# Kernel optimization log

Hardware: AMD Instinct MI355X
Metric: run time of the kernel (lower is better)

## Reference

```python
import jax, jax.numpy as jnp
import numpy as np

D_MODEL, D_K, D_V, H, GRID = 512, 64, 64, 8, 196
B = 4


def setup_inputs() -> dict:
    key = jax.random.key(0)
    ks = jax.random.split(key, 12)
    s = 0.02
    return {
        "queries": jax.random.normal(ks[0], (B, GRID, D_MODEL), jnp.float32),
        "keys": jax.random.normal(ks[1], (B, GRID, D_MODEL), jnp.float32),
        "values": jax.random.normal(ks[2], (B, GRID, D_MODEL), jnp.float32),
        "Wq": jax.random.normal(ks[3], (H * D_K, D_MODEL), jnp.float32) * s,
        "bq": jnp.zeros((H * D_K,), jnp.float32),
        "Wk": jax.random.normal(ks[4], (H * D_K, D_MODEL), jnp.float32) * s,
        "bk": jnp.zeros((H * D_K,), jnp.float32),
        "Wv": jax.random.normal(ks[5], (H * D_V, D_MODEL), jnp.float32) * s,
        "bv": jnp.zeros((H * D_V,), jnp.float32),
        "Wo": jax.random.normal(ks[6], (D_MODEL, H * D_V), jnp.float32) * s,
        "bo": jnp.zeros((D_MODEL,), jnp.float32),
        "scale": jnp.ones((1, H, GRID, GRID), jnp.float32) / np.sqrt(D_K).astype(np.float32),
    }


def reference(queries, keys, values, Wq, bq, Wk, bk, Wv, bv, Wo, bo, scale):
    b, nq, _ = queries.shape
    nk = values.shape[1]
    # linear projections (torch nn.Linear: x @ W.T + b)
    q_sig = queries @ Wq.T + bq          # (b, nq, h*dk)
    k_p = keys @ Wk.T + bk               # (b, nk, h*dk)
    v_p = values @ Wv.T + bv             # (b, nk, h*dv)
    # elementwise q*k interaction (b, nq, nk, h*dk)
    att_e = q_sig[:, :, None, :] * k_p[:, None, :, :]
    # sigmoid-gated values
    v_g = jax.nn.sigmoid(att_e) * v_p[:, None, :, :]
    v = v_g.reshape(b, nq, nk, H, D_K).transpose(0, 3, 1, 2, 4)      # (b,h,nq,nk,dk)
    att = att_e.reshape(b, nq, nk, H, D_K).transpose(0, 3, 1, 2, 4)  # (b,h,nq,nk,dk)
    att = att.sum(-1) * scale            # (b,h,nq,nk)
    p = jax.nn.softmax(att, axis=-1)     # dropout is identity in eval mode
    # (att.unsqueeze(-2) @ v).squeeze(-2)
    image = jnp.einsum("bhqk,bhqkd->bhqd", p, v)
    image = image.transpose(0, 2, 1, 3).reshape(b, nq, H * D_V)
    out = image @ Wo.T + bo              # (b, nq, d_model)
    out = jax.nn.sigmoid(q_sig * out) * out
    return out
```

## Files before the change

kernel.cpp:

```cpp
#include <hip/hip_runtime.h>
#include <hip/hip_bf16.h>
#include <math.h>

#define NQ 196
#define BATCH 4
#define HD 512
#define NH 8
#define DK 64
#define MROWS 784
#define MPAD 832

typedef __attribute__((ext_vector_type(8))) short short8;
typedef __attribute__((ext_vector_type(4))) short short4v;
typedef __attribute__((ext_vector_type(4))) float float4v;

__device__ __forceinline__ float b2f(short s) {
  return __uint_as_float(((unsigned)(unsigned short)s) << 16);
}
__device__ __forceinline__ short f2b(float x) {
  return __builtin_bit_cast(short, __float2bfloat16(x));
}
__device__ __forceinline__ float fexp2(float x) {
  float r; asm("v_exp_f32 %0, %1" : "=v"(r) : "v"(x)); return r;
}
__device__ __forceinline__ float frcp(float x) {
  float r; asm("v_rcp_f32 %0, %1" : "=v"(r) : "v"(x)); return r;
}
__device__ __forceinline__ void cvt4(float4 v, short4v& hi, short4v& lo) {
  float x[4] = {v.x, v.y, v.z, v.w};
  #pragma unroll
  for (int i = 0; i < 4; ++i) {
    hi[i] = f2b(x[i]);
    lo[i] = f2b(x[i] - b2f(hi[i]));
  }
}
__device__ __forceinline__ void gload_lds16(const void* g, void* l) {
  __builtin_amdgcn_global_load_lds(
      (const __attribute__((address_space(1))) unsigned int*)g,
      (__attribute__((address_space(3))) unsigned int*)l, 16, 0, 0);
}

struct WSplitArgs { const float* src[7]; short* hi[7]; short* lo[7]; int nblk[7]; };

__global__ __launch_bounds__(256)
void wsplit_kernel(WSplitArgs a) {
  int b = blockIdx.x, seg = 0;
  while (seg < 6 && b >= a.nblk[seg]) { b -= a.nblk[seg]; ++seg; }
  const size_t off = (size_t)b * 2048 + (size_t)threadIdx.x * 8;
  const float* src = a.src[seg] + off;
  float4 v0 = *(const float4*)(src);
  float4 v1 = *(const float4*)(src + 4);
  short4v h0, l0, h1, l1;
  cvt4(v0, h0, l0); cvt4(v1, h1, l1);
  short8 vh = {h0[0],h0[1],h0[2],h0[3],h1[0],h1[1],h1[2],h1[3]};
  short8 vl = {l0[0],l0[1],l0[2],l0[3],l1[0],l1[1],l1[2],l1[3]};
  *(short8*)(a.hi[seg] + off) = vh;
  *(short8*)(a.lo[seg] + off) = vl;
}

struct GemmArgs {
  const short* Ah[3]; const short* Al[3];
  const short* Bh[3]; const short* Bl[3];
  const float* bias[3];
  float* Cf[3]; short* Ch[3]; short* Cl[3]; const float* gate[3];
};

__global__ __launch_bounds__(512)
void mgemm(GemmArgs p, int M, int N, int K) {
  const int z = blockIdx.z;
  const short* __restrict__ Ah = p.Ah[z];
  const short* __restrict__ Al = p.Al[z];
  const short* __restrict__ Bh = p.Bh[z];
  const short* __restrict__ Bl = p.Bl[z];

  __shared__ short smem[32768];
  const int t = threadIdx.x;
  const int ln = t & 63, lm = ln & 15, quad = ln >> 4;
  const int w = t >> 6;
  const int wm = w >> 1, wn = w & 1;
  const int m0 = blockIdx.x << 6, n0 = blockIdx.y << 6;

  const int sr = t >> 3;
  const int sc = ((t & 7) ^ (sr & 7)) << 3;
  const short* gA_h = Ah + (size_t)(m0 + sr) * K + sc;
  const short* gA_l = Al + (size_t)(m0 + sr) * K + sc;
  const short* gB_h = Bh + (size_t)(n0 + sr) * K + sc;
  const short* gB_l = Bl + (size_t)(n0 + sr) * K + sc;
  const int ldst = t * 8;

  float4v acc0 = {0.f,0.f,0.f,0.f}, acc1 = {0.f,0.f,0.f,0.f};

  gload_lds16(gA_h, &smem[0     + ldst]);
  gload_lds16(gA_l, &smem[4096  + ldst]);
  gload_lds16(gB_h, &smem[8192  + ldst]);
  gload_lds16(gB_l, &smem[12288 + ldst]);

  const int NT = K >> 6;
  const int ar = (wm << 4) + lm;
  const int br0 = (wn << 5) + lm, br1 = br0 + 16;
  const int swz = (lm & 7) << 3;

  for (int kt = 0; kt < NT; ++kt) {
    const int buf = kt & 1;
    __syncthreads();
    if (kt + 1 < NT) {
      const int kb = (kt + 1) << 6;
      short* nb = &smem[(buf ^ 1) << 14];
      gload_lds16(gA_h + kb, nb + 0     + ldst);
      gload_lds16(gA_l + kb, nb + 4096  + ldst);
      gload_lds16(gB_h + kb, nb + 8192  + ldst);
      gload_lds16(gB_l + kb, nb + 12288 + ldst);
    }
    const short* Sb = &smem[buf << 14];
    #pragma unroll
    for (int h = 0; h < 2; ++h) {
      const int c = (h << 5) + (quad << 3);
      const int cs = c ^ swz;
      short8 a_h = *(const short8*)&Sb[         ar  * 64 + cs];
      short8 a_l = *(const short8*)&Sb[4096  +  ar  * 64 + cs];
      short8 b0h = *(const short8*)&Sb[8192  +  br0 * 64 + cs];
      short8 b0l = *(const short8*)&Sb[12288 +  br0 * 64 + cs];
      short8 b1h = *(const short8*)&Sb[8192  +  br1 * 64 + cs];
      short8 b1l = *(const short8*)&Sb[12288 +  br1 * 64 + cs];
      acc0 = __builtin_amdgcn_mfma_f32_16x16x32_bf16(a_h, b0h, acc0, 0,0,0);
      acc0 = __builtin_amdgcn_mfma_f32_16x16x32_bf16(a_h, b0l, acc0, 0,0,0);
      acc0 = __builtin_amdgcn_mfma_f32_16x16x32_bf16(a_l, b0h, acc0, 0,0,0);
      acc1 = __builtin_amdgcn_mfma_f32_16x16x32_bf16(a_h, b1h, acc1, 0,0,0);
      acc1 = __builtin_amdgcn_mfma_f32_16x16x32_bf16(a_h, b1l, acc1, 0,0,0);
      acc1 = __builtin_amdgcn_mfma_f32_16x16x32_bf16(a_l, b1h, acc1, 0,0,0);
    }
  }

  const float* bias = p.bias[z];
  const float* gate = p.gate[z];
  float* Cf = p.Cf[z]; short* Ch = p.Ch[z]; short* Cl = p.Cl[z];
  #pragma unroll
  for (int nf = 0; nf < 2; ++nf) {
    const float4v a = nf ? acc1 : acc0;
    const int n = n0 + (wn << 5) + (nf << 4) + lm;
    const float bv = bias[n];
    #pragma unroll
    for (int r = 0; r < 4; ++r) {
      const int m = m0 + (wm << 4) + (quad << 2) + r;
      if (m < M) {
        float c = a[r] + bv;
        if (gate) {
          const float qg = gate[(size_t)m * N + n];
          c = __fdividef(c, 1.f + __expf(-qg * c));
        }
        if (Cf) Cf[(size_t)m * N + n] = c;
        if (Ch) {
          const short hi = f2b(c);
          Ch[(size_t)m * N + n] = hi;
          Cl[(size_t)m * N + n] = f2b(c - b2f(hi));
        }
      }
    }
  }
}

__global__ __launch_bounds__(512)
void attn_fused(const short* __restrict__ qsh, const short* __restrict__ qsl,
                const short* __restrict__ ksh, const short* __restrict__ ksl,
                const float* __restrict__ qsg, const float* __restrict__ kpg,
                const float* __restrict__ vpg, const float* __restrict__ scg,
                short* __restrict__ imgh, short* __restrict__ imgl) {
  const int q0 = blockIdx.x * 16;
  const int h  = blockIdx.y;
  const int b  = blockIdx.z;
  const int t  = threadIdx.x;
  const int w = t >> 6, ln = t & 63;
  const int lm = ln & 15, quad = ln >> 4;
  const float L2E = 1.4426950408889634f;

  __shared__ __align__(16) float S[16][212];
  __shared__ float R[8][16][64];

  const size_t abase = ((size_t)(b * NQ) + q0 + lm) * HD + h * DK + (quad << 3);
  short8 ah0 = *(const short8*)(qsh + abase);
  short8 ah1 = *(const short8*)(qsh + abase + 32);
  short8 al0 = *(const short8*)(qsl + abase);
  short8 al1 = *(const short8*)(qsl + abase + 32);

  for (int nt = w; nt < 13; nt += 8) {
    const size_t bbase = ((size_t)(b * NQ) + nt * 16 + lm) * HD + h * DK + (quad << 3);
    short8 bh0 = *(const short8*)(ksh + bbase);
    short8 bh1 = *(const short8*)(ksh + bbase + 32);
    short8 bl0 = *(const short8*)(ksl + bbase);
    short8 bl1 = *(const short8*)(ksl + bbase + 32);
    float4v acc = {0.f, 0.f, 0.f, 0.f};
    acc = __builtin_amdgcn_mfma_f32_16x16x32_bf16(ah0, bh0, acc, 0,0,0);
    acc = __builtin_amdgcn_mfma_f32_16x16x32_bf16(ah1, bh1, acc, 0,0,0);
    acc = __builtin_amdgcn_mfma_f32_16x16x32_bf16(ah0, bl0, acc, 0,0,0);
    acc = __builtin_amdgcn_mfma_f32_16x16x32_bf16(ah1, bl1, acc, 0,0,0);
    acc = __builtin_amdgcn_mfma_f32_16x16x32_bf16(al0, bh0, acc, 0,0,0);
    acc = __builtin_amdgcn_mfma_f32_16x16x32_bf16(al1, bh1, acc, 0,0,0);
    #pragma unroll
    for (int r = 0; r < 4; ++r)
      S[(quad << 2) + r][nt * 16 + lm] = acc[r];
  }
  __syncthreads();

  for (int i = 0; i < 2; ++i) {
    const int rr = (w << 1) + i;
    const int q = q0 + rr;
    const bool qok = q < NQ;
    const float* srow = scg + ((size_t)h * NQ + (qok ? q : 0)) * NQ;
    float att[4];
    #pragma unroll
    for (int j = 0; j < 4; ++j) {
      const int c = ln + (j << 6);
      att[j] = -1e30f;
      if (c < NQ) att[j] = S[rr][c] * srow[c] * L2E;
    }
    float m = fmaxf(fmaxf(att[0], att[1]), fmaxf(att[2], att[3]));
    #pragma unroll
    for (int off = 32; off; off >>= 1) m = fmaxf(m, __shfl_xor(m, off, 64));
    float e[4], s = 0.f;
    #pragma unroll
    for (int j = 0; j < 4; ++j) { e[j] = fexp2(att[j] - m); s += e[j]; }
    #pragma unroll
    for (int off = 32; off; off >>= 1) s += __shfl_xor(s, off, 64);
    const float rinv = __fdividef(1.f, s);
    #pragma unroll
    for (int j = 0; j < 4; ++j) {
      const int c = ln + (j << 6);
      if (c < NQ) S[rr][c] = e[j] * rinv;
    }
  }
  __syncthreads();

  const int d = ln;
  const int kg = w;
  const int kbeg = kg * 24;
  const int kend = (kg == 7) ? 196 : kbeg + 24;
  const float LOG2E = 1.4426950408889634f;

  float nqs[16];
  #pragma unroll
  for (int qi = 0; qi < 16; ++qi) {
    const int row = min(b * NQ + q0 + qi, MROWS - 1);
    nqs[qi] = -qsg[(size_t)row * HD + h * DK + d] * LOG2E;
  }
  const float* kp = kpg + ((size_t)(b * NQ)) * HD + h * DK + d;
  const float* vp = vpg + ((size_t)(b * NQ)) * HD + h * DK + d;

  float acc[16];
  #pragma unroll
  for (int qi = 0; qi < 16; ++qi) acc[qi] = 0.f;

  for (int k = kbeg; k < kend; k += 4) {
    const float kv0 = kp[(size_t)(k + 0) * HD];
    const float kv1 = kp[(size_t)(k + 1) * HD];
    const float kv2 = kp[(size_t)(k + 2) * HD];
    const float kv3 = kp[(size_t)(k + 3) * HD];
    const float vv0 = vp[(size_t)(k + 0) * HD];
    const float vv1 = vp[(size_t)(k + 1) * HD];
    const float vv2 = vp[(size_t)(k + 2) * HD];
    const float vv3 = vp[(size_t)(k + 3) * HD];
    #pragma unroll
    for (int qi = 0; qi < 16; ++qi) {
      const float4 s4 = *(const float4*)&S[qi][k];
      acc[qi] += s4.x * (vv0 * frcp(1.f + fexp2(nqs[qi] * kv0)));
      acc[qi] += s4.y * (vv1 * frcp(1.f + fexp2(nqs[qi] * kv1)));
      acc[qi] += s4.z * (vv2 * frcp(1.f + fexp2(nqs[qi] * kv2)));
      acc[qi] += s4.w * (vv3 * frcp(1.f + fexp2(nqs[qi] * kv3)));
    }
  }
  #pragma unroll
  for (int qi = 0; qi < 16; ++qi) R[kg][qi][d] = acc[qi];
  __syncthreads();

  #pragma unroll
  for (int j = 0; j < 2; ++j) {
    const int idx = t + (j << 9);
    const int qi = idx >> 6, dd = idx & 63;
    const int q = q0 + qi;
    if (q < NQ) {
      float s = 0.f;
      #pragma unroll
      for (int kk = 0; kk < 8; ++kk) s += R[kk][qi][dd];
      const size_t o = ((size_t)(b * NQ) + q) * HD + h * DK + dd;
      const short hi = f2b(s);
      imgh[o] = hi;
      imgl[o] = f2b(s - b2f(hi));
    }
  }
}

extern "C" void kernel_launch(void* const* d_in, const int* in_sizes, int n_in,
                              void* d_out, int out_size, void* d_ws, size_t ws_size,
                              hipStream_t stream) {
  const float* queries = (const float*)d_in[0];
  const float* keys    = (const float*)d_in[1];
  const float* values  = (const float*)d_in[2];
  const float* Wq = (const float*)d_in[3];
  const float* bq = (const float*)d_in[4];
  const float* Wk = (const float*)d_in[5];
  const float* bk = (const float*)d_in[6];
  const float* Wv = (const float*)d_in[7];
  const float* bv = (const float*)d_in[8];
  const float* Wo = (const float*)d_in[9];
  const float* bo = (const float*)d_in[10];
  const float* scale = (const float*)d_in[11];

  char* base = (char*)d_ws;
  const size_t FB = sizeof(float);
  const size_t NELF  = (size_t)MROWS * HD;
  const size_t NELPS = (size_t)MPAD * HD;
  const size_t WEL   = (size_t)HD * HD;

  size_t o = 0;
  float* q_sig = (float*)(base + o); o += NELF * FB;
  float* k_p   = (float*)(base + o); o += NELF * FB;
  float* v_p   = (float*)(base + o); o += NELF * FB;
  short* qsh = (short*)(base + o); o += NELPS * 2;
  short* qsl = (short*)(base + o); o += NELPS * 2;
  short* ksh = (short*)(base + o); o += NELPS * 2;
  short* ksl = (short*)(base + o); o += NELPS * 2;
  short* imgh = (short*)(base + o); o += NELPS * 2;
  short* imgl = (short*)(base + o); o += NELPS * 2;
  short* xqh = (short*)(base + o); o += NELPS * 2;
  short* xql = (short*)(base + o); o += NELPS * 2;
  short* xkh = (short*)(base + o); o += NELPS * 2;
  short* xkl = (short*)(base + o); o += NELPS * 2;
  short* xvh = (short*)(base + o); o += NELPS * 2;
  short* xvl = (short*)(base + o); o += NELPS * 2;
  short* Wqh = (short*)(base + o); o += WEL * 2;
  short* Wql = (short*)(base + o); o += WEL * 2;
  short* Wkh = (short*)(base + o); o += WEL * 2;
  short* Wkl = (short*)(base + o); o += WEL * 2;
  short* Wvh = (short*)(base + o); o += WEL * 2;
  short* Wvl = (short*)(base + o); o += WEL * 2;
  short* Woh = (short*)(base + o); o += WEL * 2;
  short* Wol = (short*)(base + o); o += WEL * 2;

  WSplitArgs wa;
  wa.src[0] = Wq;      wa.hi[0] = Wqh; wa.lo[0] = Wql; wa.nblk[0] = 128;
  wa.src[1] = Wk;      wa.hi[1] = Wkh; wa.lo[1] = Wkl; wa.nblk[1] = 128;
  wa.src[2] = Wv;      wa.hi[2] = Wvh; wa.lo[2] = Wvl; wa.nblk[2] = 128;
  wa.src[3] = Wo;      wa.hi[3] = Woh; wa.lo[3] = Wol; wa.nblk[3] = 128;
  wa.src[4] = queries; wa.hi[4] = xqh; wa.lo[4] = xql; wa.nblk[4] = 196;
  wa.src[5] = keys;    wa.hi[5] = xkh; wa.lo[5] = xkl; wa.nblk[5] = 196;
  wa.src[6] = values;  wa.hi[6] = xvh; wa.lo[6] = xvl; wa.nblk[6] = 196;
  wsplit_kernel<<<1100, 256, 0, stream>>>(wa);

  GemmArgs gp;
  gp.Ah[0] = xqh; gp.Al[0] = xql; gp.Bh[0] = Wqh; gp.Bl[0] = Wql; gp.bias[0] = bq;
  gp.Cf[0] = q_sig; gp.Ch[0] = qsh; gp.Cl[0] = qsl; gp.gate[0] = nullptr;
  gp.Ah[1] = xkh; gp.Al[1] = xkl; gp.Bh[1] = Wkh; gp.Bl[1] = Wkl; gp.bias[1] = bk;
  gp.Cf[1] = k_p; gp.Ch[1] = ksh; gp.Cl[1] = ksl; gp.gate[1] = nullptr;
  gp.Ah[2] = xvh; gp.Al[2] = xvl; gp.Bh[2] = Wvh; gp.Bl[2] = Wvl; gp.bias[2] = bv;
  gp.Cf[2] = v_p; gp.Ch[2] = nullptr; gp.Cl[2] = nullptr; gp.gate[2] = nullptr;
  mgemm<<<dim3(MPAD/64, HD/64, 3), 512, 0, stream>>>(gp, MROWS, HD, HD);

  attn_fused<<<dim3(13, NH, BATCH), 512, 0, stream>>>(
      qsh, qsl, ksh, ksl, q_sig, k_p, v_p, scale, imgh, imgl);

  GemmArgs go;
  go.Ah[0] = imgh; go.Al[0] = imgl; go.Bh[0] = Woh; go.Bl[0] = Wol; go.bias[0] = bo;
  go.Cf[0] = (float*)d_out; go.Ch[0] = nullptr; go.Cl[0] = nullptr; go.gate[0] = q_sig;
  for (int i = 1; i < 3; ++i) {
    go.Ah[i] = nullptr; go.Al[i] = nullptr; go.Bh[i] = nullptr; go.Bl[i] = nullptr;
    go.bias[i] = nullptr; go.Cf[i] = nullptr; go.Ch[i] = nullptr; go.Cl[i] = nullptr;
    go.gate[i] = nullptr;
  }
  mgemm<<<dim3(MPAD/64, HD/64, 1), 512, 0, stream>>>(go, MROWS, HD, HD);
}
```

Before: 138.4 us.

## Fuse split, projections, attention and output GEMM into one cooperative persistent kernel

Replaces four kernel launches (the weight/input bf16 hi/lo split, the QKV GEMM, attention and the output GEMM) with a single cooperative persistent kernel that separates phases with grid.sync. The fp32 inputs and weights are now loaded directly and converted to bf16 hi/lo in registers before the LDS store, which removes the separate split pass and its intermediate global traffic. Work items are distributed over 256 blocks with grid-stride loops. In exchange, register-side conversion sits on the GEMM critical path, two grid-wide barriers are added, and each weight tile is now re-split by every block that uses it.

Measured after the change: 318.9 us. 130% more time.

```diff
diff --git a/kernel.cpp b/kernel.cpp
--- a/kernel.cpp
+++ b/kernel.cpp
@@ -1,6 +1,9 @@
 #include <hip/hip_runtime.h>
 #include <hip/hip_bf16.h>
+#include <hip/hip_cooperative_groups.h>
 #include <math.h>
+
+namespace cg = cooperative_groups;
 
 #define NQ 196
 #define BATCH 4
@@ -9,6 +12,7 @@
 #define DK 64
 #define MROWS 784
 #define MPAD 832
+#define NBLK 256
 
 typedef __attribute__((ext_vector_type(8))) short short8;
 typedef __attribute__((ext_vector_type(4))) short short4v;
@@ -33,6 +37,12 @@
     hi[i] = f2b(x[i]);
     lo[i] = f2b(x[i] - b2f(hi[i]));
   }
+}
+__device__ __forceinline__ void cvt8(float4 v0, float4 v1, short8& hi, short8& lo) {
+  short4v h0, l0, h1, l1;
+  cvt4(v0, h0, l0); cvt4(v1, h1, l1);
+  hi = short8{h0[0],h0[1],h0[2],h0[3],h1[0],h1[1],h1[2],h1[3]};
+  lo = short8{l0[0],l0[1],l0[2],l0[3],l1[0],l1[1],l1[2],l1[3]};
 }
 __device__ __forceinline__ void gload_lds16(const void* g, void* l) {
   __builtin_amdgcn_global_load_lds(
@@ -40,141 +50,181 @@
       (__attribute__((address_space(3))) unsigned int*)l, 16, 0, 0);
 }
 
-struct WSplitArgs { const float* src[7]; short* hi[7]; short* lo[7]; int nblk[7]; };
-
-__global__ __launch_bounds__(256)
-void wsplit_kernel(WSplitArgs a) {
-  int b = blockIdx.x, seg = 0;
-  while (seg < 6 && b >= a.nblk[seg]) { b -= a.nblk[seg]; ++seg; }
-  const size_t off = (size_t)b * 2048 + (size_t)threadIdx.x * 8;
-  const float* src = a.src[seg] + off;
-  float4 v0 = *(const float4*)(src);
-  float4 v1 = *(const float4*)(src + 4);
-  short4v h0, l0, h1, l1;
-  cvt4(v0, h0, l0); cvt4(v1, h1, l1);
-  short8 vh = {h0[0],h0[1],h0[2],h0[3],h1[0],h1[1],h1[2],h1[3]};
-  short8 vl = {l0[0],l0[1],l0[2],l0[3],l1[0],l1[1],l1[2],l1[3]};
-  *(short8*)(a.hi[seg] + off) = vh;
-  *(short8*)(a.lo[seg] + off) = vl;
-}
-
-struct GemmArgs {
-  const short* Ah[3]; const short* Al[3];
-  const short* Bh[3]; const short* Bl[3];
-  const float* bias[3];
-  float* Cf[3]; short* Ch[3]; short* Cl[3]; const float* gate[3];
+struct MegaArgs {
+  const float* X[3]; const float* W[3]; const float* bias[3];
+  float* Cf[3]; short* Ch[3]; short* Cl[3];
+  const float* Wo; const float* bo; const float* scale;
+  short* imgh; short* imgl; float* out;
 };
 
-__global__ __launch_bounds__(512)
-void mgemm(GemmArgs p, int M, int N, int K) {
-  const int z = blockIdx.z;
-  const short* __restrict__ Ah = p.Ah[z];
-  const short* __restrict__ Al = p.Al[z];
-  const short* __restrict__ Bh = p.Bh[z];
-  const short* __restrict__ Bl = p.Bl[z];
-
-  __shared__ short smem[32768];
+
+__device__ __forceinline__ void frag_mfma(const short* Sb, int ar, int br0, int br1,
+                                          int quad, int swz,
+                                          float4v& acc0, float4v& acc1) {
+  #pragma unroll
+  for (int h2 = 0; h2 < 2; ++h2) {
+    const int c = (h2 << 5) + (quad << 3);
+    const int cs = c ^ swz;
+    short8 a_h = *(const short8*)&Sb[         ar  * 64 + cs];
+    short8 a_l = *(const short8*)&Sb[4096  +  ar  * 64 + cs];
+    short8 b0h = *(const short8*)&Sb[8192  +  br0 * 64 + cs];
+    short8 b0l = *(const short8*)&Sb[12288 +  br0 * 64 + cs];
+    short8 b1h = *(const short8*)&Sb[8192  +  br1 * 64 + cs];
+    short8 b1l = *(const short8*)&Sb[12288 +  br1 * 64 + cs];
+    acc0 = __builtin_amdgcn_mfma_f32_16x16x32_bf16(a_h, b0h, acc0, 0,0,0);
+    acc0 = __builtin_amdgcn_mfma_f32_16x16x32_bf16(a_h, b0l, acc0, 0,0,0);
+    acc0 = __builtin_amdgcn_mfma_f32_16x16x32_bf16(a_l, b0h, acc0, 0,0,0);
+    acc1 = __builtin_amdgcn_mfma_f32_16x16x32_bf16(a_h, b1h, acc1, 0,0,0);
+    acc1 = __builtin_amdgcn_mfma_f32_16x16x32_bf16(a_h, b1l, acc1, 0,0,0);
+    acc1 = __builtin_amdgcn_mfma_f32_16x16x32_bf16(a_l, b1h, acc1, 0,0,0);
+  }
+}
+
+__device__ void gemm_proj_item(const MegaArgs& a, int z, int m0, int n0, short* smem) {
+  const float* __restrict__ X = a.X[z];
+  const float* __restrict__ W = a.W[z];
   const int t = threadIdx.x;
   const int ln = t & 63, lm = ln & 15, quad = ln >> 4;
-  const int w = t >> 6;
-  const int wm = w >> 1, wn = w & 1;
-  const int m0 = blockIdx.x << 6, n0 = blockIdx.y << 6;
+  const int w = t >> 6, wm = w >> 1, wn = w & 1;
 
   const int sr = t >> 3;
-  const int sc = ((t & 7) ^ (sr & 7)) << 3;
-  const short* gA_h = Ah + (size_t)(m0 + sr) * K + sc;
-  const short* gA_l = Al + (size_t)(m0 + sr) * K + sc;
-  const short* gB_h = Bh + (size_t)(n0 + sr) * K + sc;
-  const short* gB_l = Bl + (size_t)(n0 + sr) * K + sc;
-  const int ldst = t * 8;
-
+  const int cg = (t & 7) << 3;
+  const int wIdx = sr * 64 + (cg ^ ((sr & 7) << 3));
+  const float* gA = X + (size_t)min(m0 + sr, MROWS - 1) * HD;
+  const float* gB = W + (size_t)(n0 + sr) * HD;
+
+  float4 ra0, ra1, rb0, rb1;
   float4v acc0 = {0.f,0.f,0.f,0.f}, acc1 = {0.f,0.f,0.f,0.f};
-
-  gload_lds16(gA_h, &smem[0     + ldst]);
-  gload_lds16(gA_l, &smem[4096  + ldst]);
-  gload_lds16(gB_h, &smem[8192  + ldst]);
-  gload_lds16(gB_l, &smem[12288 + ldst]);
-
-  const int NT = K >> 6;
   const int ar = (wm << 4) + lm;
   const int br0 = (wn << 5) + lm, br1 = br0 + 16;
   const int swz = (lm & 7) << 3;
 
-  for (int kt = 0; kt < NT; ++kt) {
+  ra0 = *(const float4*)(gA + cg);     ra1 = *(const float4*)(gA + cg + 4);
+  rb0 = *(const float4*)(gB + cg);     rb1 = *(const float4*)(gB + cg + 4);
+  {
+    short8 hi, lo;
+    cvt8(ra0, ra1, hi, lo);
+    *(short8*)&smem[0    + wIdx] = hi;  *(short8*)&smem[4096  + wIdx] = lo;
+    cvt8(rb0, rb1, hi, lo);
+    *(short8*)&smem[8192 + wIdx] = hi;  *(short8*)&smem[12288 + wIdx] = lo;
+  }
+
+  for (int kt = 0; kt < 8; ++kt) {
     const int buf = kt & 1;
     __syncthreads();
-    if (kt + 1 < NT) {
+    if (kt < 7) {
       const int kb = (kt + 1) << 6;
-      short* nb = &smem[(buf ^ 1) << 14];
-      gload_lds16(gA_h + kb, nb + 0     + ldst);
-      gload_lds16(gA_l + kb, nb + 4096  + ldst);
-      gload_lds16(gB_h + kb, nb + 8192  + ldst);
-      gload_lds16(gB_l + kb, nb + 12288 + ldst);
-    }
-    const short* Sb = &smem[buf << 14];
-    #pragma unroll
-    for (int h = 0; h < 2; ++h) {
-      const int c = (h << 5) + (quad << 3);
-      const int cs = c ^ swz;
-      short8 a_h = *(const short8*)&Sb[         ar  * 64 + cs];
-      short8 a_l = *(const short8*)&Sb[4096  +  ar  * 64 + cs];
-      short8 b0h = *(const short8*)&Sb[8192  +  br0 * 64 + cs];
-      short8 b0l = *(const short8*)&Sb[12288 +  br0 * 64 + cs];
-      short8 b1h = *(const short8*)&Sb[8192  +  br1 * 64 + cs];
-      short8 b1l = *(const short8*)&Sb[12288 +  br1 * 64 + cs];
-      acc0 = __builtin_amdgcn_mfma_f32_16x16x32_bf16(a_h, b0h, acc0, 0,0,0);
-      acc0 = __builtin_amdgcn_mfma_f32_16x16x32_bf16(a_h, b0l, acc0, 0,0,0);
-      acc0 = __builtin_amdgcn_mfma_f32_16x16x32_bf16(a_l, b0h, acc0, 0,0,0);
-      acc1 = __builtin_amdgcn_mfma_f32_16x16x32_bf16(a_h, b1h, acc1, 0,0,0);
-      acc1 = __builtin_amdgcn_mfma_f32_16x16x32_bf16(a_h, b1l, acc1, 0,0,0);
-      acc1 = __builtin_amdgcn_mfma_f32_16x16x32_bf16(a_l, b1h, acc1, 0,0,0);
-    }
-  }
-
-  const float* bias = p.bias[z];
-  const float* gate = p.gate[z];
-  float* Cf = p.Cf[z]; short* Ch = p.Ch[z]; short* Cl = p.Cl[z];
+      ra0 = *(const float4*)(gA + kb + cg);  ra1 = *(const float4*)(gA + kb + cg + 4);
+      rb0 = *(const float4*)(gB + kb + cg);  rb1 = *(const float4*)(gB + kb + cg + 4);
+    }
+    const short* Sb = smem + (buf << 14);
+    frag_mfma(Sb, ar, br0, br1, quad, swz, acc0, acc1);
+    if (kt < 7) {
+      short* Nb = smem + ((buf ^ 1) << 14);
+      short8 hi, lo;
+      cvt8(ra0, ra1, hi, lo);
+      *(short8*)&Nb[0    + wIdx] = hi;  *(short8*)&Nb[4096  + wIdx] = lo;
+      cvt8(rb0, rb1, hi, lo);
+      *(short8*)&Nb[8192 + wIdx] = hi;  *(short8*)&Nb[12288 + wIdx] = lo;
+    }
+  }
+
+  const float* bias = a.bias[z];
+  float* Cf = a.Cf[z]; short* Ch = a.Ch[z]; short* Cl = a.Cl[z];
   #pragma unroll
   for (int nf = 0; nf < 2; ++nf) {
-    const float4v a = nf ? acc1 : acc0;
+    const float4v av = nf ? acc1 : acc0;
     const int n = n0 + (wn << 5) + (nf << 4) + lm;
     const float bv = bias[n];
     #pragma unroll
     for (int r = 0; r < 4; ++r) {
       const int m = m0 + (wm << 4) + (quad << 2) + r;
-      if (m < M) {
-        float c = a[r] + bv;
-        if (gate) {
-          const float qg = gate[(size_t)m * N + n];
-          c = __fdividef(c, 1.f + __expf(-qg * c));
-        }
-        if (Cf) Cf[(size_t)m * N + n] = c;
-        if (Ch) {
-          const short hi = f2b(c);
-          Ch[(size_t)m * N + n] = hi;
-          Cl[(size_t)m * N + n] = f2b(c - b2f(hi));
-        }
+      const float c = av[r] + bv;
+      Cf[(size_t)m * HD + n] = c;
+      if (Ch) {
+        const short hi = f2b(c);
+        Ch[(size_t)m * HD + n] = hi;
+        Cl[(size_t)m * HD + n] = f2b(c - b2f(hi));
       }
     }
   }
 }
 
-__global__ __launch_bounds__(512)
-void attn_fused(const short* __restrict__ qsh, const short* __restrict__ qsl,
-                const short* __restrict__ ksh, const short* __restrict__ ksl,
-                const float* __restrict__ qsg, const float* __restrict__ kpg,
-                const float* __restrict__ vpg, const float* __restrict__ scg,
-                short* __restrict__ imgh, short* __restrict__ imgl) {
-  const int q0 = blockIdx.x * 16;
-  const int h  = blockIdx.y;
-  const int b  = blockIdx.z;
-  const int t  = threadIdx.x;
+__device__ void gemm_out_item(const MegaArgs& a, int m0, int n0, short* smem) {
+  const int t = threadIdx.x;
+  const int ln = t & 63, lm = ln & 15, quad = ln >> 4;
+  const int w = t >> 6, wm = w >> 1, wn = w & 1;
+
+  const int sr = t >> 3;
+  const int cg = (t & 7) << 3;
+  const int ssc = cg ^ ((sr & 7) << 3);
+  const short* gAh = a.imgh + (size_t)(m0 + sr) * HD + ssc;
+  const short* gAl = a.imgl + (size_t)(m0 + sr) * HD + ssc;
+  const int ldst = t * 8;
+  const float* gB = a.Wo + (size_t)(n0 + sr) * HD;
+  const int wIdx = sr * 64 + ssc;
+
+  float4 rb0, rb1;
+  float4v acc0 = {0.f,0.f,0.f,0.f}, acc1 = {0.f,0.f,0.f,0.f};
+  const int ar = (wm << 4) + lm;
+  const int br0 = (wn << 5) + lm, br1 = br0 + 16;
+  const int swz = (lm & 7) << 3;
+
+  gload_lds16(gAh, &smem[0    + ldst]);
+  gload_lds16(gAl, &smem[4096 + ldst]);
+  rb0 = *(const float4*)(gB + cg);  rb1 = *(const float4*)(gB + cg + 4);
+  {
+    short8 hi, lo; cvt8(rb0, rb1, hi, lo);
+    *(short8*)&smem[8192 + wIdx] = hi;  *(short8*)&smem[12288 + wIdx] = lo;
+  }
+
+  for (int kt = 0; kt < 8; ++kt) {
+    const int buf = kt & 1;
+    __syncthreads();
+    if (kt < 7) {
+      const int kb = (kt + 1) << 6;
+      short* Nb = smem + ((buf ^ 1) << 14);
+      gload_lds16(gAh + kb, &Nb[0    + ldst]);
+      gload_lds16(gAl + kb, &Nb[4096 + ldst]);
+      rb0 = *(const float4*)(gB + kb + cg);  rb1 = *(const float4*)(gB + kb + cg + 4);
+    }
+    const short* Sb = smem + (buf << 14);
+    frag_mfma(Sb, ar, br0, br1, quad, swz, acc0, acc1);
+    if (kt < 7) {
+      short* Nb = smem + ((buf ^ 1) << 14);
+      short8 hi, lo; cvt8(rb0, rb1, hi, lo);
+      *(short8*)&Nb[8192 + wIdx] = hi;  *(short8*)&Nb[12288 + wIdx] = lo;
+    }
+  }
+
+  const float* q_sig = a.Cf[0];
+  #pragma unroll
+  for (int nf = 0; nf < 2; ++nf) {
+    const float4v av = nf ? acc1 : acc0;
+    const int n = n0 + (wn << 5) + (nf << 4) + lm;
+    const float bv = a.bo[n];
+    #pragma unroll
+    for (int r = 0; r < 4; ++r) {
+      const int m = m0 + (wm << 4) + (quad << 2) + r;
+      if (m < MROWS) {
+        float c = av[r] + bv;
+        const float qg = q_sig[(size_t)m * HD + n];
+        c = __fdividef(c, 1.f + __expf(-qg * c));
+        a.out[(size_t)m * HD + n] = c;
+      }
+    }
+  }
+}
+
+__device__ void attn_item(const MegaArgs& a, int q0, int h, int b, short* smem) {
+  float* S = (float*)smem;
+  float* R = (float*)smem + 16 * 212;
+  const int t = threadIdx.x;
   const int w = t >> 6, ln = t & 63;
   const int lm = ln & 15, quad = ln >> 4;
   const float L2E = 1.4426950408889634f;
-
-  __shared__ __align__(16) float S[16][212];
-  __shared__ float R[8][16][64];
+  const short* qsh = a.Ch[0]; const short* qsl = a.Cl[0];
+  const short* ksh = a.Ch[1]; const short* ksl = a.Cl[1];
 
   const size_t abase = ((size_t)(b * NQ) + q0 + lm) * HD + h * DK + (quad << 3);
   short8 ah0 = *(const short8*)(qsh + abase);
@@ -197,7 +247,7 @@
     acc = __builtin_amdgcn_mfma_f32_16x16x32_bf16(al1, bh1, acc, 0,0,0);
     #pragma unroll
     for (int r = 0; r < 4; ++r)
-      S[(quad << 2) + r][nt * 16 + lm] = acc[r];
+      S[((quad << 2) + r) * 212 + nt * 16 + lm] = acc[r];
   }
   __syncthreads();
 
@@ -205,13 +255,13 @@
     const int rr = (w << 1) + i;
     const int q = q0 + rr;
     const bool qok = q < NQ;
-    const float* srow = scg + ((size_t)h * NQ + (qok ? q : 0)) * NQ;
+    const float* srow = a.scale + ((size_t)h * NQ + (qok ? q : 0)) * NQ;
     float att[4];
     #pragma unroll
     for (int j = 0; j < 4; ++j) {
       const int c = ln + (j << 6);
       att[j] = -1e30f;
-      if (c < NQ) att[j] = S[rr][c] * srow[c] * L2E;
+      if (c < NQ) att[j] = S[rr * 212 + c] * srow[c] * L2E;
     }
     float m = fmaxf(fmaxf(att[0], att[1]), fmaxf(att[2], att[3]));
     #pragma unroll
@@ -225,7 +275,7 @@
     #pragma unroll
     for (int j = 0; j < 4; ++j) {
       const int c = ln + (j << 6);
-      if (c < NQ) S[rr][c] = e[j] * rinv;
+      if (c < NQ) S[rr * 212 + c] = e[j] * rinv;
     }
   }
   __syncthreads();
@@ -240,10 +290,10 @@
   #pragma unroll
   for (int qi = 0; qi < 16; ++qi) {
     const int row = min(b * NQ + q0 + qi, MROWS - 1);
-    nqs[qi] = -qsg[(size_t)row * HD + h * DK + d] * LOG2E;
-  }
-  const float* kp = kpg + ((size_t)(b * NQ)) * HD + h * DK + d;
-  const float* vp = vpg + ((size_t)(b * NQ)) * HD + h * DK + d;
+    nqs[qi] = -a.Cf[0][(size_t)row * HD + h * DK + d] * LOG2E;
+  }
+  const float* kp = a.Cf[1] + ((size_t)(b * NQ)) * HD + h * DK + d;
+  const float* vp = a.Cf[2] + ((size_t)(b * NQ)) * HD + h * DK + d;
 
   float acc[16];
   #pragma unroll
@@ -260,7 +310,7 @@
     const float vv3 = vp[(size_t)(k + 3) * HD];
     #pragma unroll
     for (int qi = 0; qi < 16; ++qi) {
-      const float4 s4 = *(const float4*)&S[qi][k];
+      const float4 s4 = *(const float4*)&S[qi * 212 + k];
       acc[qi] += s4.x * (vv0 * frcp(1.f + fexp2(nqs[qi] * kv0)));
       acc[qi] += s4.y * (vv1 * frcp(1.f + fexp2(nqs[qi] * kv1)));
       acc[qi] += s4.z * (vv2 * frcp(1.f + fexp2(nqs[qi] * kv2)));
@@ -268,7 +318,7 @@
     }
   }
   #pragma unroll
-  for (int qi = 0; qi < 16; ++qi) R[kg][qi][d] = acc[qi];
+  for (int qi = 0; qi < 16; ++qi) R[(kg * 16 + qi) * 64 + d] = acc[qi];
   __syncthreads();
 
   #pragma unroll
@@ -279,12 +329,39 @@
     if (q < NQ) {
       float s = 0.f;
       #pragma unroll
-      for (int kk = 0; kk < 8; ++kk) s += R[kk][qi][dd];
+      for (int kk = 0; kk < 8; ++kk) s += R[(kk * 16 + qi) * 64 + dd];
       const size_t o = ((size_t)(b * NQ) + q) * HD + h * DK + dd;
       const short hi = f2b(s);
-      imgh[o] = hi;
-      imgl[o] = f2b(s - b2f(hi));
-    }
+      a.imgh[o] = hi;
+      a.imgl[o] = f2b(s - b2f(hi));
+    }
+  }
+  __syncthreads();
+}
+
+__global__ __launch_bounds__(512, 1)
+void mega_kernel(MegaArgs a) {
+  cg::grid_group grid = cg::this_grid();
+  __shared__ __align__(16) short smem[32768];
+
+  for (int it = blockIdx.x; it < 312; it += gridDim.x) {
+    const int z = it / 104, mn = it % 104;
+    gemm_proj_item(a, z, (mn % 13) << 6, (mn / 13) << 6, smem);
+    __syncthreads();
+  }
+  __threadfence();
+  grid.sync();
+
+  for (int it = blockIdx.x; it < 416; it += gridDim.x) {
+    const int qt = it % 13, hb = it / 13;
+    attn_item(a, qt << 4, hb >> 2, hb & 3, smem);
+  }
+  __threadfence();
+  grid.sync();
+
+  for (int it = blockIdx.x; it < 104; it += gridDim.x) {
+    gemm_out_item(a, (it % 13) << 6, (it / 13) << 6, smem);
+    __syncthreads();
   }
 }
 
@@ -305,65 +382,31 @@
   const float* scale = (const float*)d_in[11];
 
   char* base = (char*)d_ws;
-  const size_t FB = sizeof(float);
-  const size_t NELF  = (size_t)MROWS * HD;
   const size_t NELPS = (size_t)MPAD * HD;
-  const size_t WEL   = (size_t)HD * HD;
 
   size_t o = 0;
-  float* q_sig = (float*)(base + o); o += NELF * FB;
-  float* k_p   = (float*)(base + o); o += NELF * FB;
-  float* v_p   = (float*)(base + o); o += NELF * FB;
+  float* q_sig = (float*)(base + o); o += NELPS * 4;
+  float* k_p   = (float*)(base + o); o += NELPS * 4;
+  float* v_p   = (float*)(base + o); o += NELPS * 4;
   short* qsh = (short*)(base + o); o += NELPS * 2;
   short* qsl = (short*)(base + o); o += NELPS * 2;
   short* ksh = (short*)(base + o); o += NELPS * 2;
   short* ksl = (short*)(base + o); o += NELPS * 2;
   short* imgh = (short*)(base + o); o += NELPS * 2;
   short* imgl = (short*)(base + o); o += NELPS * 2;
-  short* xqh = (short*)(base + o); o += NELPS * 2;
-  short* xql = (short*)(base + o); o += NELPS * 2;
-  short* xkh = (short*)(base + o); o += NELPS * 2;
-  short* xkl = (short*)(base + o); o += NELPS * 2;
-  short* xvh = (short*)(base + o); o += NELPS * 2;
-  short* xvl = (short*)(base + o); o += NELPS * 2;
-  short* Wqh = (short*)(base + o); o += WEL * 2;
-  short* Wql = (short*)(base + o); o += WEL * 2;
-  short* Wkh = (short*)(base + o); o += WEL * 2;
-  short* Wkl = (short*)(base + o); o += WEL * 2;
-  short* Wvh = (short*)(base + o); o += WEL * 2;
-  short* Wvl = (short*)(base + o); o += WEL * 2;
-  short* Woh = (short*)(base + o); o += WEL * 2;
-  short* Wol = (short*)(base + o); o += WEL * 2;
-
-  WSplitArgs wa;
-  wa.src[0] = Wq;      wa.hi[0] = Wqh; wa.lo[0] = Wql; wa.nblk[0] = 128;
-  wa.src[1] = Wk;      wa.hi[1] = Wkh; wa.lo[1] = Wkl; wa.nblk[1] = 128;
-  wa.src[2] = Wv;      wa.hi[2] = Wvh; wa.lo[2] = Wvl; wa.nblk[2] = 128;
-  wa.src[3] = Wo;      wa.hi[3] = Woh; wa.lo[3] = Wol; wa.nblk[3] = 128;
-  wa.src[4] = queries; wa.hi[4] = xqh; wa.lo[4] = xql; wa.nblk[4] = 196;
-  wa.src[5] = keys;    wa.hi[5] = xkh; wa.lo[5] = xkl; wa.nblk[5] = 196;
-  wa.src[6] = values;  wa.hi[6] = xvh; wa.lo[6] = xvl; wa.nblk[6] = 196;
-  wsplit_kernel<<<1100, 256, 0, stream>>>(wa);
-
-  GemmArgs gp;
-  gp.Ah[0] = xqh; gp.Al[0] = xql; gp.Bh[0] = Wqh; gp.Bl[0] = Wql; gp.bias[0] = bq;
-  gp.Cf[0] = q_sig; gp.Ch[0] = qsh; gp.Cl[0] = qsl; gp.gate[0] = nullptr;
-  gp.Ah[1] = xkh; gp.Al[1] = xkl; gp.Bh[1] = Wkh; gp.Bl[1] = Wkl; gp.bias[1] = bk;
-  gp.Cf[1] = k_p; gp.Ch[1] = ksh; gp.Cl[1] = ksl; gp.gate[1] = nullptr;
-  gp.Ah[2] = xvh; gp.Al[2] = xvl; gp.Bh[2] = Wvh; gp.Bl[2] = Wvl; gp.bias[2] = bv;
-  gp.Cf[2] = v_p; gp.Ch[2] = nullptr; gp.Cl[2] = nullptr; gp.gate[2] = nullptr;
-  mgemm<<<dim3(MPAD/64, HD/64, 3), 512, 0, stream>>>(gp, MROWS, HD, HD);
-
-  attn_fused<<<dim3(13, NH, BATCH), 512, 0, stream>>>(
-      qsh, qsl, ksh, ksl, q_sig, k_p, v_p, scale, imgh, imgl);
-
-  GemmArgs go;
-  go.Ah[0] = imgh; go.Al[0] = imgl; go.Bh[0] = Woh; go.Bl[0] = Wol; go.bias[0] = bo;
-  go.Cf[0] = (float*)d_out; go.Ch[0] = nullptr; go.Cl[0] = nullptr; go.gate[0] = q_sig;
-  for (int i = 1; i < 3; ++i) {
-    go.Ah[i] = nullptr; go.Al[i] = nullptr; go.Bh[i] = nullptr; go.Bl[i] = nullptr;
-    go.bias[i] = nullptr; go.Cf[i] = nullptr; go.Ch[i] = nullptr; go.Cl[i] = nullptr;
-    go.gate[i] = nullptr;
-  }
-  mgemm<<<dim3(MPAD/64, HD/64, 1), 512, 0, stream>>>(go, MROWS, HD, HD);
-}
+
+  MegaArgs m;
+  m.X[0] = queries; m.X[1] = keys; m.X[2] = values;
+  m.W[0] = Wq;      m.W[1] = Wk;   m.W[2] = Wv;
+  m.bias[0] = bq;   m.bias[1] = bk; m.bias[2] = bv;
+  m.Cf[0] = q_sig;  m.Cf[1] = k_p;  m.Cf[2] = v_p;
+  m.Ch[0] = qsh; m.Cl[0] = qsl;
+  m.Ch[1] = ksh; m.Cl[1] = ksl;
+  m.Ch[2] = nullptr; m.Cl[2] = nullptr;
+  m.Wo = Wo; m.bo = bo; m.scale = scale;
+  m.imgh = imgh; m.imgl = imgl; m.out = (float*)d_out;
+
+  void* kargs[] = { &m };
+  hipLaunchCooperativeKernel((void*)mega_kernel, dim3(NBLK), dim3(512),
+                             kargs, 0, stream);
+}
```
